# Optimization experiments

Hardware: AMD Instinct MI355X
Metric: run time of the kernel (lower is better)

Reference implementation:

```python
import jax, jax.numpy as jnp
import numpy as np

B, C, N = 8, 512, 2048  # batch, channels (=size), tokens


def setup_inputs() -> dict:
    key = jax.random.key(0)
    ks = jax.random.split(key, 9)
    s = 1.0 / np.sqrt(C)
    return {
        "q": jax.random.normal(ks[0], (B, C, N), dtype=jnp.float32),
        "k": jax.random.normal(ks[1], (B, C, N), dtype=jnp.float32),
        "v": jax.random.normal(ks[2], (B, C, N), dtype=jnp.float32),
        "wq": jax.random.normal(ks[3], (C, C), dtype=jnp.float32) * s,
        "bq": jax.random.normal(ks[4], (C,), dtype=jnp.float32) * s,
        "wk": jax.random.normal(ks[5], (C, C), dtype=jnp.float32) * s,
        "bk": jax.random.normal(ks[6], (C,), dtype=jnp.float32) * s,
        "wv": jax.random.normal(ks[7], (C, C), dtype=jnp.float32) * s,
        "bv": jax.random.normal(ks[8], (C,), dtype=jnp.float32) * s,
    }


def _proj(x, w, b):
    # 1x1 conv over channels: out[b,c,n] = sum_i w[c,i] x[b,i,n] + b[c]
    return jnp.einsum('ci,bin->bcn', w, x) + b[None, :, None]


def reference(q, k, v, wq, bq, wk, bk, wv, bv):
    residual = q                                   # [B, C, N]
    qp = _proj(q, wq, bq).transpose(0, 2, 1)       # [B, N, C]
    kp = _proj(k, wk, bk).transpose(0, 2, 1)       # [B, N, C]
    vp = _proj(v, wv, bv).transpose(0, 2, 1)       # [B, N, C]
    attn = jnp.einsum('bnc,bmc->bnm', qp, kp)      # raw QK^T, no scale/softmax
    out = jnp.einsum('bnm,bmc->bnc', attn, vp)     # [B, N, C]
    return out.transpose(0, 2, 1) + residual       # [B, C, N]
```

## Files before the change

### kernel.cpp

```cpp
#include <hip/hip_runtime.h>
#include <hip/hip_bf16.h>
#include <stdint.h>

#define B_ 8
#define C_ 512
#define N_ 2048

typedef __bf16 bf16_t;
typedef bf16_t bf16x8 __attribute__((ext_vector_type(8)));
typedef bf16_t bf16x4 __attribute__((ext_vector_type(4)));
typedef float f32x4 __attribute__((ext_vector_type(4)));

__global__ __launch_bounds__(256) void cast_w_kernel(
    const float* __restrict__ w0, const float* __restrict__ w1,
    bf16_t* __restrict__ out)
{
    const float* src = (blockIdx.z == 0) ? w0 : w1;
    bf16_t* dst = out + (size_t)blockIdx.z * (C_ * C_);
    int i = (blockIdx.x * 256 + threadIdx.x) * 4;
    float4 f = *(const float4*)(src + i);
    bf16x4 o;
    o[0] = (bf16_t)f.x; o[1] = (bf16_t)f.y; o[2] = (bf16_t)f.z; o[3] = (bf16_t)f.w;
    *(bf16x4*)(dst + i) = o;
}

__global__ __launch_bounds__(256) void transpose_cast_w_kernel(
    const float* __restrict__ in, bf16_t* __restrict__ out)
{
    __shared__ bf16_t tile[64][65];
    const int i0 = blockIdx.x * 64;
    const int c0 = blockIdx.y * 64;
    const int t = threadIdx.x;
    const int cx = (t & 15) * 4;
    const int ry = t >> 4;
#pragma unroll
    for (int r = ry; r < 64; r += 16) {
        float4 f = *(const float4*)&in[(size_t)(c0 + r) * C_ + i0 + cx];
        tile[r][cx + 0] = (bf16_t)f.x;
        tile[r][cx + 1] = (bf16_t)f.y;
        tile[r][cx + 2] = (bf16_t)f.z;
        tile[r][cx + 3] = (bf16_t)f.w;
    }
    __syncthreads();
    const int c4 = (t & 15) * 4;
    const int rb = t >> 4;
#pragma unroll
    for (int r = rb; r < 64; r += 16) {
        bf16x4 o;
        o[0] = tile[c4 + 0][r];
        o[1] = tile[c4 + 1][r];
        o[2] = tile[c4 + 2][r];
        o[3] = tile[c4 + 3][r];
        *(bf16x4*)&out[(size_t)(i0 + r) * C_ + c0 + c4] = o;
    }
}

template <int EPI>
__global__ __launch_bounds__(256, 2) void proj_gemm(
    const bf16_t* __restrict__ A0, const bf16_t* __restrict__ A1,
    const float* __restrict__ X0, const float* __restrict__ X1,
    void* __restrict__ Cd0, void* __restrict__ Cd1,
    const float* __restrict__ bias0, const float* __restrict__ bias1,
    const float* __restrict__ resid, size_t sAb, int bstride)
{
    __shared__ __align__(16) bf16_t As[128 * 64];
    __shared__ __align__(16) char  Bs[128 * 128];

    const int tid  = threadIdx.x;
    const int lane = tid & 63;
    const int wave = tid >> 6;
    const int wr = wave >> 1, wc = wave & 1;
    const int half = blockIdx.z >> 3;
    const int bz = blockIdx.z & 7;
    const int m0 = blockIdx.y * 128;
    const int n0 = blockIdx.x * 128;

    const bf16_t* A = (half ? A1 : A0) + (size_t)bz * sAb;
    const float*  X = (half ? X1 : X0) + (size_t)bz * ((size_t)C_ * N_);
    const float*  bias = half ? bias1 : bias0;

    f32x4 acc[4][4];
#pragma unroll
    for (int i = 0; i < 4; ++i)
#pragma unroll
        for (int j = 0; j < 4; ++j) acc[i][j] = 0.f;

    const int srow  = tid >> 3;
    const int scolA = ((tid & 7) ^ (srow & 7)) * 8;
    const int ldsA  = tid * 16;

    const int sa  = lane >> 3;
    const int snl = wave * 32 + (lane & 7) * 4;

    float4 xf0[4], xf1[4];

    auto stage_a = [&](int t) {
        const bf16_t* ga = A + (size_t)(m0 + srow) * C_ + t * 64 + scolA;
#pragma unroll
        for (int p = 0; p < 4; ++p)
            __builtin_amdgcn_global_load_lds(
                (const __attribute__((address_space(1))) void*)(ga + (size_t)p * 32 * C_),
                (__attribute__((address_space(3))) void*)((char*)As + ldsA + p * 4096),
                16, 0, 0);
    };
    auto load_x = [&](int t) {
#pragma unroll
        for (int p = 0; p < 4; ++p) {
            const int iL = 16 * p + 2 * sa;
            const float* g0 = X + (size_t)(t * 64 + iL) * N_ + n0 + snl;
            xf0[p] = *(const float4*)g0;
            xf1[p] = *(const float4*)(g0 + N_);
        }
    };
    auto write_b = [&]() {
#pragma unroll
        for (int p = 0; p < 4; ++p) {
            const int iL = 16 * p + 2 * sa;
#pragma unroll
            for (int j = 0; j < 4; ++j) {
                const int n = snl + j;
                const int g = ((n ^ (n >> 3)) & 7) << 4;
                const int off = n * 128 + ((2 * iL) ^ g);
                union { bf16_t h[2]; uint32_t u; } pk;
                pk.h[0] = (bf16_t)((&xf0[p].x)[j]);
                pk.h[1] = (bf16_t)((&xf1[p].x)[j]);
                *(uint32_t*)(Bs + off) = pk.u;
            }
        }
    };
    auto compute = [&]() {
#pragma unroll
        for (int kk = 0; kk < 64; kk += 32) {
            bf16x8 af[4], bfr[4];
            const int kcol = kk + (lane >> 4) * 8;
            const int kc = kcol >> 3;
#pragma unroll
            for (int m = 0; m < 4; ++m) {
                const int row = wr * 64 + (lane & 15) + m * 16;
                af[m] = *(const bf16x8*)((const char*)As + row * 128 +
                                         ((kc ^ (row & 7)) << 4));
            }
#pragma unroll
            for (int n = 0; n < 4; ++n) {
                const int row = wc * 64 + (lane & 15) + n * 16;
                const int g = ((row ^ (row >> 3)) & 7) << 4;
                bfr[n] = *(const bf16x8*)(Bs + row * 128 + ((2 * kcol) ^ g));
            }
#pragma unroll
            for (int m = 0; m < 4; ++m)
#pragma unroll
                for (int n = 0; n < 4; ++n)
                    acc[m][n] = __builtin_amdgcn_mfma_f32_16x16x32_bf16(
                        af[m], bfr[n], acc[m][n], 0, 0, 0);
        }
    };

    load_x(0);
#pragma unroll
    for (int t = 0; t < 8; ++t) {
        stage_a(t);
        write_b();
        __syncthreads();
        if (t < 7) load_x(t + 1);
        compute();
        __syncthreads();
    }

    const int rj = (lane >> 4) * 4;
    const int cc = lane & 15;
    void* Csel = half ? Cd1 : Cd0;
#pragma unroll
    for (int m = 0; m < 4; ++m) {
#pragma unroll
        for (int n = 0; n < 4; ++n) {
            const int col = n0 + wc * 64 + n * 16 + cc;
            f32x4 vv = acc[m][n];
#pragma unroll
            for (int j = 0; j < 4; ++j) {
                const int row = m0 + wr * 64 + m * 16 + rj + j;
                float val = vv[j] + bias[bstride * bz + row];
                const size_t o = (size_t)bz * ((size_t)C_ * N_) + (size_t)row * N_ + col;
                if (EPI == 3) {
                    ((float*)Csel)[o] = val + resid[o];
                } else {
                    ((bf16_t*)Csel)[o] = (bf16_t)val;
                }
            }
        }
    }
}

template <int SPLITS>
__global__ __launch_bounds__(256, 2) void gemm_nt(
    const bf16_t* __restrict__ A, const bf16_t* __restrict__ Bm,
    bf16_t* __restrict__ Cout,
    int Nn, int K, size_t sA, size_t sB, size_t sC)
{
    __shared__ __align__(16) bf16_t As[128 * 64];
    __shared__ __align__(16) bf16_t Bs2[128 * 64];

    const int tid  = threadIdx.x;
    const int lane = tid & 63;
    const int wave = tid >> 6;
    const int wr = wave >> 1, wc = wave & 1;
    const int bz = blockIdx.z / SPLITS;
    const int sp = blockIdx.z % SPLITS;
    const int kbeg = sp * (K / SPLITS);
    const int nt = (K / SPLITS) / 64;

    const bf16_t* Ab = A + (size_t)bz * sA;
    const bf16_t* Bb = Bm + (size_t)bz * sB;
    const int m0 = blockIdx.y * 128;
    const int n0 = blockIdx.x * 128;

    f32x4 acc[4][4];
#pragma unroll
    for (int i = 0; i < 4; ++i)
#pragma unroll
        for (int j = 0; j < 4; ++j) acc[i][j] = 0.f;

    const int srow = tid >> 3;
    const int scol = ((tid & 7) ^ (srow & 7)) * 8;
    const int ldso = tid * 16;

    for (int t = 0; t < nt; ++t) {
        const bf16_t* ga = Ab + (size_t)(m0 + srow) * K + kbeg + t * 64 + scol;
        const bf16_t* gb = Bb + (size_t)(n0 + srow) * K + kbeg + t * 64 + scol;
#pragma unroll
        for (int p = 0; p < 4; ++p)
            __builtin_amdgcn_global_load_lds(
                (const __attribute__((address_space(1))) void*)(ga + (size_t)p * 32 * K),
                (__attribute__((address_space(3))) void*)((char*)As + ldso + p * 4096),
                16, 0, 0);
#pragma unroll
        for (int p = 0; p < 4; ++p)
            __builtin_amdgcn_global_load_lds(
                (const __attribute__((address_space(1))) void*)(gb + (size_t)p * 32 * K),
                (__attribute__((address_space(3))) void*)((char*)Bs2 + ldso + p * 4096),
                16, 0, 0);
        __syncthreads();

#pragma unroll
        for (int kk = 0; kk < 64; kk += 32) {
            bf16x8 af[4], bfr[4];
            const int kcol = kk + (lane >> 4) * 8;
            const int kc = kcol >> 3;
#pragma unroll
            for (int m = 0; m < 4; ++m) {
                const int row = wr * 64 + (lane & 15) + m * 16;
                af[m] = *(const bf16x8*)((const char*)As + row * 128 +
                                         ((kc ^ (row & 7)) << 4));
            }
#pragma unroll
            for (int n = 0; n < 4; ++n) {
                const int row = wc * 64 + (lane & 15) + n * 16;
                bfr[n] = *(const bf16x8*)((const char*)Bs2 + row * 128 +
                                          ((kc ^ (row & 7)) << 4));
            }
#pragma unroll
            for (int m = 0; m < 4; ++m)
#pragma unroll
                for (int n = 0; n < 4; ++n)
                    acc[m][n] = __builtin_amdgcn_mfma_f32_16x16x32_bf16(
                        af[m], bfr[n], acc[m][n], 0, 0, 0);
        }
        __syncthreads();
    }

    const int rj = (lane >> 4) * 4;
    const int cc = lane & 15;
#pragma unroll
    for (int m = 0; m < 4; ++m) {
#pragma unroll
        for (int n = 0; n < 4; ++n) {
            const int col = n0 + wc * 64 + n * 16 + cc;
            f32x4 vv = acc[m][n];
#pragma unroll
            for (int j = 0; j < 4; ++j) {
                const int row = m0 + wr * 64 + m * 16 + rj + j;
                Cout[(size_t)blockIdx.z * sC + (size_t)row * Nn + col] = (bf16_t)vv[j];
            }
        }
    }
}

__global__ __launch_bounds__(256) void reduce_splitk_kernel(
    const bf16_t* __restrict__ Pt, bf16_t* __restrict__ Out)
{
    const size_t sCC = (size_t)C_ * C_;
    size_t idx = ((size_t)blockIdx.x * 256 + threadIdx.x) * 8;
    size_t b = idx / sCC;
    size_t r = idx - b * sCC;
    const bf16_t* base = Pt + (b * 4) * sCC + r;
    float acc[8];
#pragma unroll
    for (int j = 0; j < 8; ++j) acc[j] = 0.f;
#pragma unroll
    for (int s = 0; s < 4; ++s) {
        bf16x8 pv = *(const bf16x8*)(base + (size_t)s * sCC);
#pragma unroll
        for (int j = 0; j < 8; ++j) acc[j] += (float)pv[j];
    }
    bf16x8 o;
#pragma unroll
    for (int j = 0; j < 8; ++j) o[j] = (bf16_t)acc[j];
    *(bf16x8*)(Out + idx) = o;
}

__global__ __launch_bounds__(256) void compute_h_kernel(
    const bf16_t* __restrict__ St, const float* __restrict__ bq,
    float* __restrict__ h)
{
    const int b = blockIdx.x;
    const int c = threadIdx.x * 2;
#pragma unroll
    for (int rr = 0; rr < 2; ++rr) {
        const bf16_t* row = St + ((size_t)b * C_ + c + rr) * C_;
        float acc = 0.f;
        for (int j = 0; j < C_; j += 8) {
            bf16x8 vv = *(const bf16x8*)(row + j);
#pragma unroll
            for (int t = 0; t < 8; ++t) acc += (float)vv[t] * bq[j + t];
        }
        h[b * C_ + c + rr] = acc;
    }
}

extern "C" void kernel_launch(void* const* d_in, const int* in_sizes, int n_in,
                              void* d_out, int out_size, void* d_ws, size_t ws_size,
                              hipStream_t stream)
{
    (void)in_sizes; (void)n_in; (void)out_size; (void)ws_size;
    const float* q  = (const float*)d_in[0];
    const float* k  = (const float*)d_in[1];
    const float* v  = (const float*)d_in[2];
    const float* wq = (const float*)d_in[3];
    const float* bq = (const float*)d_in[4];
    const float* wk = (const float*)d_in[5];
    const float* bk = (const float*)d_in[6];
    const float* wv = (const float*)d_in[7];
    const float* bv = (const float*)d_in[8];
    float* out = (float*)d_out;

    char* ws = (char*)d_ws;
    const size_t WSZ = (size_t)C_ * C_ * 2;
    const size_t TSZ = (size_t)B_ * N_ * C_ * 2;
    const size_t SCZ = (size_t)B_ * C_ * C_ * 2;
    bf16_t* Wkb  = (bf16_t*)(ws);
    bf16_t* Wvb  = (bf16_t*)(ws + WSZ);
    bf16_t* WqTb = (bf16_t*)(ws + 2 * WSZ);
    bf16_t* Pk   = (bf16_t*)(ws + 3 * WSZ);
    bf16_t* Pv   = (bf16_t*)(ws + 3 * WSZ + TSZ);
    bf16_t* Stp  = (bf16_t*)(ws + 3 * WSZ + 2 * TSZ);
    bf16_t* Hp   = (bf16_t*)(ws + 3 * WSZ + 3 * TSZ);
    bf16_t* St   = (bf16_t*)(ws + 3 * WSZ + 4 * TSZ);
    bf16_t* HT   = (bf16_t*)(ws + 3 * WSZ + 4 * TSZ + SCZ);
    float*  hb   = (float*)(ws + 3 * WSZ + 4 * TSZ + 2 * SCZ);

    const dim3 blk(256);
    const size_t sBN = (size_t)N_ * C_;
    const size_t sCC = (size_t)C_ * C_;

    cast_w_kernel<<<dim3(256, 1, 2), blk, 0, stream>>>(wk, wv, Wkb);
    transpose_cast_w_kernel<<<dim3(C_ / 64, C_ / 64), blk, 0, stream>>>(wq, WqTb);

    proj_gemm<1><<<dim3(N_ / 128, C_ / 128, 2 * B_), blk, 0, stream>>>(
        Wkb, Wvb, k, v, (void*)Pk, (void*)Pv, bk, bv, nullptr, 0, 0);

    gemm_nt<4><<<dim3(C_ / 128, C_ / 128, B_ * 4), blk, 0, stream>>>(
        Pv, Pk, Stp, C_, N_, sBN, sBN, sCC);
    reduce_splitk_kernel<<<dim3((B_ * sCC) / (256 * 8)), blk, 0, stream>>>(Stp, St);

    gemm_nt<4><<<dim3(C_ / 128, C_ / 128, B_ * 4), blk, 0, stream>>>(
        St, WqTb, Hp, C_, C_, sCC, 0, sCC);
    reduce_splitk_kernel<<<dim3((B_ * sCC) / (256 * 8)), blk, 0, stream>>>(Hp, HT);
    compute_h_kernel<<<dim3(B_), blk, 0, stream>>>(St, bq, hb);

    proj_gemm<3><<<dim3(N_ / 128, C_ / 128, B_), blk, 0, stream>>>(
        HT, HT, q, q, (void*)out, (void*)out, hb, hb, q, sCC, C_);
}
```

Measured before the change: 127.7 us.

## Compute K·Vᵀ on raw inputs and fold projection weights into small C×C GEMMs

```diff
diff --git a/kernel.cpp b/kernel.cpp
--- a/kernel.cpp
+++ b/kernel.cpp
@@ -55,29 +55,57 @@
     }
 }
 
-template <int EPI>
-__global__ __launch_bounds__(256, 2) void proj_gemm(
-    const bf16_t* __restrict__ A0, const bf16_t* __restrict__ A1,
-    const float* __restrict__ X0, const float* __restrict__ X1,
-    void* __restrict__ Cd0, void* __restrict__ Cd1,
-    const float* __restrict__ bias0, const float* __restrict__ bias1,
-    const float* __restrict__ resid, size_t sAb, int bstride)
+__global__ __launch_bounds__(256) void transpose_cast_kernel(
+    const float* __restrict__ in, bf16_t* __restrict__ out)
+{
+    __shared__ bf16_t tile[64][65];
+    const int b = blockIdx.z;
+    const float* src = in + (size_t)b * C_ * N_;
+    bf16_t* dst = out + (size_t)b * N_ * C_;
+    const int n0 = blockIdx.x * 64;
+    const int c0 = blockIdx.y * 64;
+    const int t = threadIdx.x;
+    const int cx = (t & 15) * 4;
+    const int ry = t >> 4;
+#pragma unroll
+    for (int r = ry; r < 64; r += 16) {
+        float4 f = *(const float4*)&src[(size_t)(c0 + r) * N_ + n0 + cx];
+        tile[r][cx + 0] = (bf16_t)f.x;
+        tile[r][cx + 1] = (bf16_t)f.y;
+        tile[r][cx + 2] = (bf16_t)f.z;
+        tile[r][cx + 3] = (bf16_t)f.w;
+    }
+    __syncthreads();
+    const int c4 = (t & 15) * 4;
+    const int rb = t >> 4;
+#pragma unroll
+    for (int r = rb; r < 64; r += 16) {
+        bf16x4 o;
+        o[0] = tile[c4 + 0][r];
+        o[1] = tile[c4 + 1][r];
+        o[2] = tile[c4 + 2][r];
+        o[3] = tile[c4 + 3][r];
+        *(bf16x4*)&dst[(size_t)(n0 + r) * C_ + c0 + c4] = o;
+    }
+}
+
+__global__ __launch_bounds__(256) void gemm_d(
+    const float* __restrict__ Kin, const float* __restrict__ Vin,
+    bf16_t* __restrict__ Dp, float* __restrict__ sk, float* __restrict__ sv)
 {
     __shared__ __align__(16) bf16_t As[128 * 64];
-    __shared__ __align__(16) char  Bs[128 * 128];
-
-    const int tid  = threadIdx.x;
-    const int lane = tid & 63;
-    const int wave = tid >> 6;
+    __shared__ __align__(16) bf16_t Bs[128 * 64];
+
+    const int tid = threadIdx.x, lane = tid & 63, wave = tid >> 6;
     const int wr = wave >> 1, wc = wave & 1;
-    const int half = blockIdx.z >> 3;
-    const int bz = blockIdx.z & 7;
-    const int m0 = blockIdx.y * 128;
-    const int n0 = blockIdx.x * 128;
-
-    const bf16_t* A = (half ? A1 : A0) + (size_t)bz * sAb;
-    const float*  X = (half ? X1 : X0) + (size_t)bz * ((size_t)C_ * N_);
-    const float*  bias = half ? bias1 : bias0;
+    const int bz = blockIdx.z >> 2, sp = blockIdx.z & 3;
+    const int m0 = blockIdx.y * 128, n0 = blockIdx.x * 128;
+    const float* A  = Kin + (size_t)bz * C_ * N_;
+    const float* Bv = Vin + (size_t)bz * C_ * N_;
+    const int kbeg = sp * 512;
+
+    const int srow = tid >> 1;
+    const int sc0  = (tid & 1) * 32;
 
     f32x4 acc[4][4];
 #pragma unroll
@@ -85,47 +113,41 @@
 #pragma unroll
         for (int j = 0; j < 4; ++j) acc[i][j] = 0.f;
 
-    const int srow  = tid >> 3;
-    const int scolA = ((tid & 7) ^ (srow & 7)) * 8;
-    const int ldsA  = tid * 16;
-
-    const int sa  = lane >> 3;
-    const int snl = wave * 32 + (lane & 7) * 4;
-
-    float4 xf0[4], xf1[4];
-
-    auto stage_a = [&](int t) {
-        const bf16_t* ga = A + (size_t)(m0 + srow) * C_ + t * 64 + scolA;
-#pragma unroll
-        for (int p = 0; p < 4; ++p)
-            __builtin_amdgcn_global_load_lds(
-                (const __attribute__((address_space(1))) void*)(ga + (size_t)p * 32 * C_),
-                (__attribute__((address_space(3))) void*)((char*)As + ldsA + p * 4096),
-                16, 0, 0);
+    float4 xa[8], xb[8];
+    float sumA = 0.f, sumB = 0.f;
+
+    auto load_t = [&](int t) {
+        const float* ga = A  + (size_t)(m0 + srow) * N_ + kbeg + t * 64 + sc0;
+        const float* gb = Bv + (size_t)(n0 + srow) * N_ + kbeg + t * 64 + sc0;
+#pragma unroll
+        for (int p = 0; p < 8; ++p) {
+            xa[p] = *(const float4*)(ga + 4 * p);
+            xb[p] = *(const float4*)(gb + 4 * p);
+        }
     };
-    auto load_x = [&](int t) {
-#pragma unroll
-        for (int p = 0; p < 4; ++p) {
-            const int iL = 16 * p + 2 * sa;
-            const float* g0 = X + (size_t)(t * 64 + iL) * N_ + n0 + snl;
-            xf0[p] = *(const float4*)g0;
-            xf1[p] = *(const float4*)(g0 + N_);
-        }
-    };
-    auto write_b = [&]() {
-#pragma unroll
-        for (int p = 0; p < 4; ++p) {
-            const int iL = 16 * p + 2 * sa;
+    auto write_t = [&]() {
+        if (blockIdx.x == 0) {
+#pragma unroll
+            for (int p = 0; p < 8; ++p) sumA += xa[p].x + xa[p].y + xa[p].z + xa[p].w;
+        }
+        if (blockIdx.y == 0) {
+#pragma unroll
+            for (int p = 0; p < 8; ++p) sumB += xb[p].x + xb[p].y + xb[p].z + xb[p].w;
+        }
+#pragma unroll
+        for (int h = 0; h < 4; ++h) {
+            bf16x8 pa, pb;
 #pragma unroll
             for (int j = 0; j < 4; ++j) {
-                const int n = snl + j;
-                const int g = ((n ^ (n >> 3)) & 7) << 4;
-                const int off = n * 128 + ((2 * iL) ^ g);
-                union { bf16_t h[2]; uint32_t u; } pk;
-                pk.h[0] = (bf16_t)((&xf0[p].x)[j]);
-                pk.h[1] = (bf16_t)((&xf1[p].x)[j]);
-                *(uint32_t*)(Bs + off) = pk.u;
-            }
+                pa[j]     = (bf16_t)((&xa[2 * h].x)[j]);
+                pa[j + 4] = (bf16_t)((&xa[2 * h + 1].x)[j]);
+                pb[j]     = (bf16_t)((&xb[2 * h].x)[j]);
+                pb[j + 4] = (bf16_t)((&xb[2 * h + 1].x)[j]);
+            }
+            const int c = (sc0 >> 3) + h;
+            const int off = srow * 128 + ((c ^ (srow & 7)) << 4);
+            *(bf16x8*)((char*)As + off) = pa;
+            *(bf16x8*)((char*)Bs + off) = pb;
         }
     };
     auto compute = [&]() {
@@ -143,8 +165,8 @@
 #pragma unroll
             for (int n = 0; n < 4; ++n) {
                 const int row = wc * 64 + (lane & 15) + n * 16;
-                const int g = ((row ^ (row >> 3)) & 7) << 4;
-                bfr[n] = *(const bf16x8*)(Bs + row * 128 + ((2 * kcol) ^ g));
+                bfr[n] = *(const bf16x8*)((const char*)Bs + row * 128 +
+                                          ((kc ^ (row & 7)) << 4));
             }
 #pragma unroll
             for (int m = 0; m < 4; ++m)
@@ -155,20 +177,18 @@
         }
     };
 
-    load_x(0);
-#pragma unroll
+    load_t(0);
     for (int t = 0; t < 8; ++t) {
-        stage_a(t);
-        write_b();
+        write_t();
         __syncthreads();
-        if (t < 7) load_x(t + 1);
+        if (t < 7) load_t(t + 1);
         compute();
         __syncthreads();
     }
 
     const int rj = (lane >> 4) * 4;
     const int cc = lane & 15;
-    void* Csel = half ? Cd1 : Cd0;
+    const size_t sCC = (size_t)C_ * C_;
 #pragma unroll
     for (int m = 0; m < 4; ++m) {
 #pragma unroll
@@ -178,109 +198,17 @@
 #pragma unroll
             for (int j = 0; j < 4; ++j) {
                 const int row = m0 + wr * 64 + m * 16 + rj + j;
-                float val = vv[j] + bias[bstride * bz + row];
-                const size_t o = (size_t)bz * ((size_t)C_ * N_) + (size_t)row * N_ + col;
-                if (EPI == 3) {
-                    ((float*)Csel)[o] = val + resid[o];
-                } else {
-                    ((bf16_t*)Csel)[o] = (bf16_t)val;
-                }
-            }
-        }
-    }
-}
-
-template <int SPLITS>
-__global__ __launch_bounds__(256, 2) void gemm_nt(
-    const bf16_t* __restrict__ A, const bf16_t* __restrict__ Bm,
-    bf16_t* __restrict__ Cout,
-    int Nn, int K, size_t sA, size_t sB, size_t sC)
-{
-    __shared__ __align__(16) bf16_t As[128 * 64];
-    __shared__ __align__(16) bf16_t Bs2[128 * 64];
-
-    const int tid  = threadIdx.x;
-    const int lane = tid & 63;
-    const int wave = tid >> 6;
-    const int wr = wave >> 1, wc = wave & 1;
-    const int bz = blockIdx.z / SPLITS;
-    const int sp = blockIdx.z % SPLITS;
-    const int kbeg = sp * (K / SPLITS);
-    const int nt = (K / SPLITS) / 64;
-
-    const bf16_t* Ab = A + (size_t)bz * sA;
-    const bf16_t* Bb = Bm + (size_t)bz * sB;
-    const int m0 = blockIdx.y * 128;
-    const int n0 = blockIdx.x * 128;
-
-    f32x4 acc[4][4];
-#pragma unroll
-    for (int i = 0; i < 4; ++i)
-#pragma unroll
-        for (int j = 0; j < 4; ++j) acc[i][j] = 0.f;
-
-    const int srow = tid >> 3;
-    const int scol = ((tid & 7) ^ (srow & 7)) * 8;
-    const int ldso = tid * 16;
-
-    for (int t = 0; t < nt; ++t) {
-        const bf16_t* ga = Ab + (size_t)(m0 + srow) * K + kbeg + t * 64 + scol;
-        const bf16_t* gb = Bb + (size_t)(n0 + srow) * K + kbeg + t * 64 + scol;
-#pragma unroll
-        for (int p = 0; p < 4; ++p)
-            __builtin_amdgcn_global_load_lds(
-                (const __attribute__((address_space(1))) void*)(ga + (size_t)p * 32 * K),
-                (__attribute__((address_space(3))) void*)((char*)As + ldso + p * 4096),
-                16, 0, 0);
-#pragma unroll
-        for (int p = 0; p < 4; ++p)
-            __builtin_amdgcn_global_load_lds(
-                (const __attribute__((address_space(1))) void*)(gb + (size_t)p * 32 * K),
-                (__attribute__((address_space(3))) void*)((char*)Bs2 + ldso + p * 4096),
-                16, 0, 0);
-        __syncthreads();
-
-#pragma unroll
-        for (int kk = 0; kk < 64; kk += 32) {
-            bf16x8 af[4], bfr[4];
-            const int kcol = kk + (lane >> 4) * 8;
-            const int kc = kcol >> 3;
-#pragma unroll
-            for (int m = 0; m < 4; ++m) {
-                const int row = wr * 64 + (lane & 15) + m * 16;
-                af[m] = *(const bf16x8*)((const char*)As + row * 128 +
-                                         ((kc ^ (row & 7)) << 4));
-            }
-#pragma unroll
-            for (int n = 0; n < 4; ++n) {
-                const int row = wc * 64 + (lane & 15) + n * 16;
-                bfr[n] = *(const bf16x8*)((const char*)Bs2 + row * 128 +
-                                          ((kc ^ (row & 7)) << 4));
-            }
-#pragma unroll
-            for (int m = 0; m < 4; ++m)
-#pragma unroll
-                for (int n = 0; n < 4; ++n)
-                    acc[m][n] = __builtin_amdgcn_mfma_f32_16x16x32_bf16(
-                        af[m], bfr[n], acc[m][n], 0, 0, 0);
-        }
-        __syncthreads();
-    }
-
-    const int rj = (lane >> 4) * 4;
-    const int cc = lane & 15;
-#pragma unroll
-    for (int m = 0; m < 4; ++m) {
-#pragma unroll
-        for (int n = 0; n < 4; ++n) {
-            const int col = n0 + wc * 64 + n * 16 + cc;
-            f32x4 vv = acc[m][n];
-#pragma unroll
-            for (int j = 0; j < 4; ++j) {
-                const int row = m0 + wr * 64 + m * 16 + rj + j;
-                Cout[(size_t)blockIdx.z * sC + (size_t)row * Nn + col] = (bf16_t)vv[j];
-            }
-        }
+                Dp[(size_t)blockIdx.z * sCC + (size_t)row * C_ + col] = (bf16_t)vv[j];
+            }
+        }
+    }
+    if (blockIdx.x == 0) {
+        float o = sumA + __shfl_xor(sumA, 1, 64);
+        if (!(tid & 1)) atomicAdd(&sk[bz * C_ + m0 + srow], o);
+    }
+    if (blockIdx.y == 0) {
+        float o = sumB + __shfl_xor(sumB, 1, 64);
+        if (!(tid & 1)) atomicAdd(&sv[bz * C_ + n0 + srow], o);
     }
 }
 
@@ -305,6 +233,130 @@
 #pragma unroll
     for (int j = 0; j < 8; ++j) o[j] = (bf16_t)acc[j];
     *(bf16x8*)(Out + idx) = o;
+}
+
+__global__ __launch_bounds__(256) void matvec_uw_kernel(
+    const bf16_t* __restrict__ Wvb, const bf16_t* __restrict__ Wkb,
+    const float* __restrict__ sv, const float* __restrict__ sk,
+    float* __restrict__ u, float* __restrict__ w)
+{
+    const int b2 = blockIdx.x;
+    const int b = b2 >> 1, sel = b2 & 1;
+    const bf16_t* W = sel ? Wkb : Wvb;
+    const float* s  = (sel ? sk : sv) + (size_t)b * C_;
+    float* o        = (sel ? w : u) + (size_t)b * C_;
+    const int c = threadIdx.x * 2;
+#pragma unroll
+    for (int rr = 0; rr < 2; ++rr) {
+        const bf16_t* row = W + (size_t)(c + rr) * C_;
+        float acc = 0.f;
+        for (int j = 0; j < C_; j += 8) {
+            bf16x8 vv = *(const bf16x8*)(row + j);
+#pragma unroll
+            for (int t = 0; t < 8; ++t) acc += (float)vv[t] * s[j + t];
+        }
+        o[c + rr] = acc;
+    }
+}
+
+template <int EPI>
+__global__ __launch_bounds__(256) void gemm_nt2(
+    const bf16_t* __restrict__ A, const bf16_t* __restrict__ Bm,
+    void* __restrict__ Cout, int Nn, int K, size_t sA, size_t sB, size_t sC,
+    const float* __restrict__ e0, const float* __restrict__ e1,
+    const float* __restrict__ e2, const float* __restrict__ e3,
+    const float* __restrict__ resid)
+{
+    __shared__ __align__(16) bf16_t As[128 * 64];
+    __shared__ __align__(16) bf16_t Bs[128 * 64];
+
+    const int tid = threadIdx.x, lane = tid & 63, wave = tid >> 6;
+    const int wr = wave >> 1, wc = wave & 1;
+    const int bz = blockIdx.z;
+    const bf16_t* Ab = A + (size_t)bz * sA;
+    const bf16_t* Bb = Bm + (size_t)bz * sB;
+    const int m0 = blockIdx.y * 128, n0 = blockIdx.x * 128;
+
+    f32x4 acc[4][4];
+#pragma unroll
+    for (int i = 0; i < 4; ++i)
+#pragma unroll
+        for (int j = 0; j < 4; ++j) acc[i][j] = 0.f;
+
+    const int srow = tid >> 3;
+    const int scol = ((tid & 7) ^ (srow & 7)) * 8;
+    const int ldso = tid * 16;
+    const int nt = K / 64;
+
+    for (int t = 0; t < nt; ++t) {
+        const bf16_t* ga = Ab + (size_t)(m0 + srow) * K + t * 64 + scol;
+        const bf16_t* gb = Bb + (size_t)(n0 + srow) * K + t * 64 + scol;
+#pragma unroll
+        for (int p = 0; p < 4; ++p)
+            __builtin_amdgcn_global_load_lds(
+                (const __attribute__((address_space(1))) void*)(ga + (size_t)p * 32 * K),
+                (__attribute__((address_space(3))) void*)((char*)As + ldso + p * 4096),
+                16, 0, 0);
+#pragma unroll
+        for (int p = 0; p < 4; ++p)
+            __builtin_amdgcn_global_load_lds(
+                (const __attribute__((address_space(1))) void*)(gb + (size_t)p * 32 * K),
+                (__attribute__((address_space(3))) void*)((char*)Bs + ldso + p * 4096),
+                16, 0, 0);
+        __syncthreads();
+
+#pragma unroll
+        for (int kk = 0; kk < 64; kk += 32) {
+            bf16x8 af[4], bfr[4];
+            const int kcol = kk + (lane >> 4) * 8;
+            const int kc = kcol >> 3;
+#pragma unroll
+            for (int m = 0; m < 4; ++m) {
+                const int row = wr * 64 + (lane & 15) + m * 16;
+                af[m] = *(const bf16x8*)((const char*)As + row * 128 +
+                                         ((kc ^ (row & 7)) << 4));
+            }
+#pragma unroll
+            for (int n = 0; n < 4; ++n) {
+                const int row = wc * 64 + (lane & 15) + n * 16;
+                bfr[n] = *(const bf16x8*)((const char*)Bs + row * 128 +
+                                          ((kc ^ (row & 7)) << 4));
+            }
+#pragma unroll
+            for (int m = 0; m < 4; ++m)
+#pragma unroll
+                for (int n = 0; n < 4; ++n)
+                    acc[m][n] = __builtin_amdgcn_mfma_f32_16x16x32_bf16(
+                        af[m], bfr[n], acc[m][n], 0, 0, 0);
+        }
+        __syncthreads();
+    }
+
+    const int rj = (lane >> 4) * 4;
+    const int cc = lane & 15;
+#pragma unroll
+    for (int m = 0; m < 4; ++m) {
+#pragma unroll
+        for (int n = 0; n < 4; ++n) {
+            const int col = n0 + wc * 64 + n * 16 + cc;
+            f32x4 vv = acc[m][n];
+#pragma unroll
+            for (int j = 0; j < 4; ++j) {
+                const int row = m0 + wr * 64 + m * 16 + rj + j;
+                float val = vv[j];
+                if (EPI == 1)
+                    val += e0[bz * C_ + row] * e1[col] +
+                           e2[row] * (e3[bz * C_ + col] + 2048.0f * e1[col]);
+                if (EPI == 2) {
+                    float* op = (float*)Cout + (size_t)bz * sC + (size_t)row * Nn + col;
+                    *op = val + e0[bz * C_ + row] +
+                          resid[(size_t)bz * sC + (size_t)row * Nn + col];
+                } else {
+                    ((bf16_t*)Cout)[(size_t)bz * sC + (size_t)row * Nn + col] = (bf16_t)val;
+                }
+            }
+        }
+    }
 }
 
 __global__ __launch_bounds__(256) void compute_h_kernel(
@@ -346,36 +398,49 @@
     const size_t WSZ = (size_t)C_ * C_ * 2;
     const size_t TSZ = (size_t)B_ * N_ * C_ * 2;
     const size_t SCZ = (size_t)B_ * C_ * C_ * 2;
-    bf16_t* Wkb  = (bf16_t*)(ws);
-    bf16_t* Wvb  = (bf16_t*)(ws + WSZ);
-    bf16_t* WqTb = (bf16_t*)(ws + 2 * WSZ);
-    bf16_t* Pk   = (bf16_t*)(ws + 3 * WSZ);
-    bf16_t* Pv   = (bf16_t*)(ws + 3 * WSZ + TSZ);
-    bf16_t* Stp  = (bf16_t*)(ws + 3 * WSZ + 2 * TSZ);
-    bf16_t* Hp   = (bf16_t*)(ws + 3 * WSZ + 3 * TSZ);
-    bf16_t* St   = (bf16_t*)(ws + 3 * WSZ + 4 * TSZ);
-    bf16_t* HT   = (bf16_t*)(ws + 3 * WSZ + 4 * TSZ + SCZ);
-    float*  hb   = (float*)(ws + 3 * WSZ + 4 * TSZ + 2 * SCZ);
+    const size_t VSZ = (size_t)B_ * C_ * 4;
+    size_t off = 0;
+    bf16_t* Wkb  = (bf16_t*)(ws + off); off += WSZ;
+    bf16_t* Wvb  = (bf16_t*)(ws + off); off += WSZ;
+    bf16_t* WqTb = (bf16_t*)(ws + off); off += WSZ;
+    bf16_t* qT   = (bf16_t*)(ws + off); off += TSZ;
+    bf16_t* Dp   = (bf16_t*)(ws + off); off += TSZ;
+    bf16_t* D    = (bf16_t*)(ws + off); off += SCZ;
+    bf16_t* P1   = (bf16_t*)(ws + off); off += SCZ;
+    bf16_t* St   = (bf16_t*)(ws + off); off += SCZ;
+    bf16_t* HT   = (bf16_t*)(ws + off); off += SCZ;
+    float*  skv  = (float*)(ws + off);  off += 2 * VSZ;
+    float*  uu   = (float*)(ws + off);  off += VSZ;
+    float*  wwv  = (float*)(ws + off);  off += VSZ;
+    float*  hb   = (float*)(ws + off);  off += VSZ;
+    float*  sk   = skv;
+    float*  sv   = skv + (size_t)B_ * C_;
 
     const dim3 blk(256);
     const size_t sBN = (size_t)N_ * C_;
     const size_t sCC = (size_t)C_ * C_;
 
+    hipMemsetAsync(skv, 0, 2 * VSZ, stream);
+
     cast_w_kernel<<<dim3(256, 1, 2), blk, 0, stream>>>(wk, wv, Wkb);
     transpose_cast_w_kernel<<<dim3(C_ / 64, C_ / 64), blk, 0, stream>>>(wq, WqTb);
-
-    proj_gemm<1><<<dim3(N_ / 128, C_ / 128, 2 * B_), blk, 0, stream>>>(
-        Wkb, Wvb, k, v, (void*)Pk, (void*)Pv, bk, bv, nullptr, 0, 0);
-
-    gemm_nt<4><<<dim3(C_ / 128, C_ / 128, B_ * 4), blk, 0, stream>>>(
-        Pv, Pk, Stp, C_, N_, sBN, sBN, sCC);
-    reduce_splitk_kernel<<<dim3((B_ * sCC) / (256 * 8)), blk, 0, stream>>>(Stp, St);
-
-    gemm_nt<4><<<dim3(C_ / 128, C_ / 128, B_ * 4), blk, 0, stream>>>(
-        St, WqTb, Hp, C_, C_, sCC, 0, sCC);
-    reduce_splitk_kernel<<<dim3((B_ * sCC) / (256 * 8)), blk, 0, stream>>>(Hp, HT);
+    transpose_cast_kernel<<<dim3(N_ / 64, C_ / 64, B_), blk, 0, stream>>>(q, qT);
+
+    gemm_d<<<dim3(C_ / 128, C_ / 128, B_ * 4), blk, 0, stream>>>(k, v, Dp, sk, sv);
+    reduce_splitk_kernel<<<dim3((B_ * sCC) / (256 * 8)), blk, 0, stream>>>(Dp, D);
+
+    matvec_uw_kernel<<<dim3(2 * B_), blk, 0, stream>>>(Wvb, Wkb, sv, sk, uu, wwv);
+
+    gemm_nt2<0><<<dim3(C_ / 128, C_ / 128, B_), blk, 0, stream>>>(
+        Wvb, D, (void*)P1, C_, C_, 0, sCC, sCC, nullptr, nullptr, nullptr, nullptr, nullptr);
+
+    gemm_nt2<1><<<dim3(C_ / 128, C_ / 128, B_), blk, 0, stream>>>(
+        P1, Wkb, (void*)St, C_, C_, sCC, 0, sCC, uu, bk, bv, wwv, nullptr);
+
     compute_h_kernel<<<dim3(B_), blk, 0, stream>>>(St, bq, hb);
-
-    proj_gemm<3><<<dim3(N_ / 128, C_ / 128, B_), blk, 0, stream>>>(
-        HT, HT, q, q, (void*)out, (void*)out, hb, hb, q, sCC, C_);
-}
+    gemm_nt2<0><<<dim3(C_ / 128, C_ / 128, B_), blk, 0, stream>>>(
+        St, WqTb, (void*)HT, C_, C_, sCC, 0, sCC, nullptr, nullptr, nullptr, nullptr, nullptr);
+
+    gemm_nt2<2><<<dim3(N_ / 128, C_ / 128, B_), blk, 0, stream>>>(
+        HT, qT, (void*)out, N_, C_, sCC, sBN, sBN, hb, nullptr, nullptr, nullptr, q);
+}
```

New measurement: 178.6 us. +39.9%, slower.
